# Kernel tuning notes

Measured on AMD Instinct MI355X. Metric: run time of the kernel, lower is better.

Reference implementation:

```python
import jax, jax.numpy as jnp
import numpy as np
from jax.scipy.linalg import solve_triangular

L_SUB = 16          # subarray length (init arg L)
DL = 0.05           # diagonal loading factor


def setup_inputs() -> dict:
    key = jax.random.key(0)
    k0, k1, k2 = jax.random.split(key, 3)
    B, C, NS, NZ, NX = 2, 128, 1024, 256, 128
    rf = jax.random.normal(k0, (B, C, NS), jnp.float32)
    t0 = jnp.zeros((B,), jnp.float32)
    d_tx = jax.random.uniform(k1, (B, NZ, NX), dtype=jnp.float32)
    d_rx = jax.random.uniform(k2, (C, NZ, NX), dtype=jnp.float32)
    fs = jnp.float32((NS - 1) / 2.0)   # keeps sample positions in [0, NS-1]
    f0 = jnp.float32(5.0)              # unused by forward (kept for signature parity)
    c0 = jnp.float32(1.0)
    apod = jnp.ones((C,), jnp.float32) # unused by forward
    return dict(rf=rf, t0=t0, d_tx=d_tx, d_rx=d_rx, fs=fs, f0=f0, c0=c0, apod=apod)


def _aligned_signals(rf, t0, d_tx, d_rx, fs, c0):
    """Bilinear (1-D linear) resample of rf at per-pixel delays.
    Equivalent to torch grid_sample(mode='bilinear', padding_mode='border',
    align_corners=True) where the grid x-coord is samples*2/(NS-1)-1."""
    B, C, NS = rf.shape
    _, NZ, NX = d_tx.shape
    # samples: [B, C, NZ, NX] fractional sample index into rf
    samples = fs * ((d_tx[:, None, :, :] + d_rx[None, :, :, :]) / c0
                    + t0[:, None, None, None])
    pos = jnp.clip(samples, 0.0, NS - 1.0)          # border padding
    i0 = jnp.floor(pos).astype(jnp.int32)
    i1 = jnp.minimum(i0 + 1, NS - 1)
    frac = pos - i0.astype(pos.dtype)
    sig = rf.reshape(B * C, NS)
    i0f = i0.reshape(B * C, NZ * NX)
    i1f = i1.reshape(B * C, NZ * NX)
    v0 = jnp.take_along_axis(sig, i0f, axis=1).reshape(B, C, NZ, NX)
    v1 = jnp.take_along_axis(sig, i1f, axis=1).reshape(B, C, NZ, NX)
    return v0 * (1.0 - frac) + v1 * frac


def reference(rf, t0, d_tx, d_rx, fs, f0, c0, apod):
    B, C, NS = rf.shape
    _, NZ, NX = d_tx.shape
    M = C - L_SUB + 1  # number of subarrays (113)
    aligned = _aligned_signals(rf, t0, d_tx, d_rx, fs, c0)  # [B, C, NZ, NX]
    # per-pixel channel vectors: [P, C], P = B*NZ*NX
    xf = aligned.transpose(0, 2, 3, 1).reshape(-1, C)
    # subarray gather: S[p, m, l] = xf[p, m + l]  -> [P, M, L]
    idx = jnp.arange(M)[:, None] + jnp.arange(L_SUB)[None, :]
    S = xf[:, idx]
    # avg_pool1d(kernel=M, stride=1) over channels == mean over subarray axis
    x = S.mean(axis=1)                                  # [P, L]
    # spatially-smoothed covariance: R = S^T S / M, symmetrized
    R = jnp.einsum('pml,pmk->plk', S, S) / M
    R = 0.5 * (R + R.transpose(0, 2, 1))
    # diagonal loading: R += dl * (trace/L) * I
    delta = jnp.trace(R, axis1=-2, axis2=-1) / L_SUB    # [P]
    R = R + (DL * delta)[:, None, None] * jnp.eye(L_SUB, dtype=R.dtype)
    # Cholesky solve R u = 1
    Lc = jnp.linalg.cholesky(R)
    rhs = jnp.ones((R.shape[0], L_SUB, 1), R.dtype)
    y1 = solve_triangular(Lc, rhs, lower=True)
    u = solve_triangular(Lc, y1, lower=True, trans=1)[..., 0]  # [P, L]
    # MVDR weights (steering a = ones) and beamformed output
    denom = jnp.sum(u, axis=-1, keepdims=True) + 1e-10
    w = u / denom
    y = jnp.sum(w * x, axis=-1)                         # [P]
    return y.reshape(B, NZ, NX)
```

## Files before the change

kernel.cpp:

```cpp
#include <hip/hip_runtime.h>


namespace {

constexpr int kB  = 2;
constexpr int kC  = 128;
constexpr int kNS = 1024;
constexpr int kNZ = 256;
constexpr int kNX = 128;
constexpr int kZX = kNZ * kNX;
constexpr int kHalfC = 64;
constexpr int kRows = 4;
constexpr int kBufF = 2 * kRows * kNS;
constexpr int kTPB = 256;

__device__ __host__ constexpr int tri(int l, int k) {
  return l * 16 - (l * (l - 1)) / 2 + (k - l);
}

typedef __attribute__((address_space(1))) const void gconst_t;
typedef __attribute__((address_space(3))) void ldsv_t;

__device__ __forceinline__ void g2l16(const float* g, float* l) {
  __builtin_amdgcn_global_load_lds((gconst_t*)g, (ldsv_t*)l, 16, 0, 0);
}

__device__ __forceinline__ void stage_step(const float* __restrict__ rfb,
                                           float* tbuf, int q, int wave,
                                           int lane) {
  const int h = wave >> 1;
  const int woff = (wave & 1) * 2048;
  const float* gsrc = rfb + (size_t)(h * kHalfC + q * kRows) * kNS;
  float* ldst = tbuf + h * (kRows * kNS);
#pragma unroll
  for (int i = 0; i < 8; ++i)
    g2l16(gsrc + woff + i * 256 + lane * 4, ldst + woff + i * 256);
}

__device__ __forceinline__ void load_drx4(const float* __restrict__ drxp,
                                          int cbase, float (&d)[kRows]) {
#pragma unroll
  for (int r = 0; r < kRows; ++r)
    d[r] = drxp[(size_t)(cbase + r) * kZX];
}

template <int PH, bool HEAD>
__device__ __forceinline__ void compute4(
    const float* rows, const float (&drx)[kRows], float kk, float base,
    float (&F)[16], float (&win)[16], float (&head)[16], float& Sall) {
#pragma unroll
  for (int r = 0; r < kRows; ++r) {
    const int t = PH + r;
    float pos = fmaf(kk, drx[r], base);
    pos = fminf(fmaxf(pos, 0.0f), 1023.0f);
    int i0 = (int)pos;
    i0 = min(i0, kNS - 2);
    float frac = pos - (float)i0;
    const float* p = rows + r * kNS + i0;
    float v0 = p[0];
    float v1 = p[1];
    float v = fmaf(frac, v1 - v0, v0);
    Sall += v;
    F[0] = fmaf(v, v, F[0]);
    if constexpr (HEAD) {
#pragma unroll
      for (int d = 1; d <= t; ++d) F[d] = fmaf(v, win[t - d], F[d]);
      head[t] = v;
    } else {
#pragma unroll
      for (int d = 1; d < 16; ++d) F[d] = fmaf(v, win[(t - d) & 15], F[d]);
    }
    win[t] = v;
  }
}

#define STEP(Q, PH, HEADF, CUR, NXT)                                       \
  do {                                                                     \
    if ((Q) + 1 < 16) {                                                    \
      stage_step(rfb, tile[((Q) + 1) & 1], (Q) + 1, wave, lane);           \
      load_drx4(drxp, ((Q) + 1) * kRows, NXT);                             \
    }                                                                      \
    compute4<PH, HEADF>(tile[(Q) & 1] + half * (kRows * kNS), CUR, kk,     \
                        base, F, win, head, Sall);                         \
    __syncthreads();                                                       \
  } while (0)

__global__ __launch_bounds__(kTPB, 2) void mvb_fused_kernel(
    const float* __restrict__ rf, const float* __restrict__ t0,
    const float* __restrict__ d_tx, const float* __restrict__ d_rx,
    const float* __restrict__ fs_p, const float* __restrict__ c0_p,
    float* __restrict__ out) {
  __shared__ float tile[2][kBufF];

  const int tid = threadIdx.x;
  const int lane = tid & 63;
  const int wave = tid >> 6;
  const int half = tid >> 7;
  const int px = tid & 127;
  const int z = blockIdx.x & (kNZ - 1);
  const int b = blockIdx.x >> 8;
  const int pix = (int)((size_t)b * kZX + z * kNX + px);

  const float fs = fs_p[0];
  const float c0 = c0_p[0];
  const float kk = fs / c0;
  const float base = fs * (d_tx[pix] / c0 + t0[b]);

  const float* rfb = rf + (size_t)b * kC * kNS;
  const float* drxp =
      d_rx + (size_t)half * kHalfC * kZX + (size_t)z * kNX + px;

  float F[16], win[16], head[16];
  float Sall = 0.0f;
#pragma unroll
  for (int i = 0; i < 16; ++i) F[i] = 0.0f;

  float drxA[kRows], drxB[kRows];

  stage_step(rfb, tile[0], 0, wave, lane);
  load_drx4(drxp, 0, drxA);
  __syncthreads();

  STEP(0, 0, true, drxA, drxB);
  STEP(1, 4, true, drxB, drxA);
  STEP(2, 8, true, drxA, drxB);
  STEP(3, 12, true, drxB, drxA);
#pragma unroll 1
  for (int g = 1; g < 4; ++g) {
    const int q = g * 4;
    STEP(q + 0, 0, false, drxA, drxB);
    STEP(q + 1, 4, false, drxB, drxA);
    STEP(q + 2, 8, false, drxA, drxB);
    STEP(q + 3, 12, false, drxB, drxA);
  }

  float* xch = tile[0];
  if (half == 0) {
#pragma unroll
    for (int i = 0; i < 16; ++i) xch[i * 128 + px] = F[i];
#pragma unroll
    for (int i = 0; i < 16; ++i) xch[(16 + i) * 128 + px] = win[i];
#pragma unroll
    for (int i = 0; i < 16; ++i) xch[(32 + i) * 128 + px] = head[i];
    xch[48 * 128 + px] = Sall;
  }
  __syncthreads();
  if (half == 0) return;

  float hlo[16];
  {
    float wlo[16];
#pragma unroll
    for (int i = 0; i < 16; ++i) wlo[i] = xch[(16 + i) * 128 + px];
#pragma unroll
    for (int i = 0; i < 16; ++i) hlo[i] = xch[(32 + i) * 128 + px];
    Sall += xch[48 * 128 + px];
    F[0] += xch[0 * 128 + px];
#pragma unroll
    for (int d = 1; d < 16; ++d) {
      float s = xch[d * 128 + px];
#pragma unroll
      for (int i = 0; i < d; ++i) s = fmaf(head[i], wlo[16 - d + i], s);
      F[d] += s;
    }
  }

  float Ru[136];
#pragma unroll
  for (int d = 0; d < 16; ++d) {
    float t0s = 0.0f;
#pragma unroll
    for (int i = d + 1; i < 16; ++i) t0s = fmaf(win[i - d], win[i], t0s);
    Ru[tri(0, d)] = F[d] - t0s;
#pragma unroll
    for (int l = 1; l < 16 - d; ++l)
      Ru[tri(l, l + d)] = Ru[tri(l - 1, l - 1 + d)] -
                          hlo[l - 1] * hlo[l - 1 + d] +
                          win[l] * win[l + d];
  }

  float tr = 0.0f;
#pragma unroll
  for (int l = 0; l < 16; ++l) tr += Ru[tri(l, l)];
  const float dl = tr * (0.05f / 16.0f);
#pragma unroll
  for (int l = 0; l < 16; ++l) Ru[tri(l, l)] += dl;

  float X[16];
  {
    float s = Sall;
#pragma unroll
    for (int i = 1; i < 16; ++i) s -= win[i];
    X[0] = s;
#pragma unroll
    for (int l = 1; l < 16; ++l) X[l] = X[l - 1] - hlo[l - 1] + win[l];
  }

  float inv[16];
#pragma unroll
  for (int j = 0; j < 16; ++j) {
    float d = Ru[tri(j, j)];
#pragma unroll
    for (int p = 0; p < j; ++p) d = fmaf(-Ru[tri(p, j)], Ru[tri(p, j)], d);
    inv[j] = rsqrtf(d);
#pragma unroll
    for (int i = j + 1; i < 16; ++i) {
      float s = Ru[tri(j, i)];
#pragma unroll
      for (int p = 0; p < j; ++p) s = fmaf(-Ru[tri(p, i)], Ru[tri(p, j)], s);
      Ru[tri(j, i)] = s * inv[j];
    }
  }

  float yv[16];
#pragma unroll
  for (int i = 0; i < 16; ++i) {
    float s = 1.0f;
#pragma unroll
    for (int j = 0; j < i; ++j) s = fmaf(-Ru[tri(j, i)], yv[j], s);
    yv[i] = s * inv[i];
  }
  float u[16];
#pragma unroll
  for (int i = 15; i >= 0; --i) {
    float s = yv[i];
#pragma unroll
    for (int j = i + 1; j < 16; ++j) s = fmaf(-Ru[tri(i, j)], u[j], s);
    u[i] = s * inv[i];
  }

  float su = 0.0f, dot = 0.0f;
#pragma unroll
  for (int i = 0; i < 16; ++i) {
    su += u[i];
    dot = fmaf(u[i], X[i], dot);
  }
  out[pix] = dot / (113.0f * su + 1e-10f);
}

}

extern "C" void kernel_launch(void* const* d_in, const int* in_sizes, int n_in,
                              void* d_out, int out_size, void* d_ws,
                              size_t ws_size, hipStream_t stream) {
  const float* rf   = (const float*)d_in[0];
  const float* t0   = (const float*)d_in[1];
  const float* d_tx = (const float*)d_in[2];
  const float* d_rx = (const float*)d_in[3];
  const float* fs   = (const float*)d_in[4];
  const float* c0   = (const float*)d_in[6];
  float* out = (float*)d_out;

  hipLaunchKernelGGL(mvb_fused_kernel, dim3(kB * kNZ), dim3(kTPB), 0, stream,
                     rf, t0, d_tx, d_rx, fs, c0, out);
}
```

Before: 97.66 us.

## Replace block-wide double buffering with per-wave 4-deep LDS ring and waitcnt pipelining

Each wave now stages its own rf rows into a private 4-slot LDS ring using async global-to-LDS loads, three rows ahead. It synchronises with explicit vmcnt/lgkmcnt waits instead of a __syncthreads after every 4-row step. All 64 d_rx values are preloaded into registers up front. Launch bounds drop to 1 block per CU, trading occupancy and a larger register footprint for removing the per-step block barriers.

Result: slower. 100.7 us (+3.2%).

```diff
diff --git a/kernel.cpp b/kernel.cpp
--- a/kernel.cpp
+++ b/kernel.cpp
@@ -9,9 +9,6 @@
 constexpr int kNZ = 256;
 constexpr int kNX = 128;
 constexpr int kZX = kNZ * kNX;
-constexpr int kHalfC = 64;
-constexpr int kRows = 4;
-constexpr int kBufF = 2 * kRows * kNS;
 constexpr int kTPB = 256;
 
 __device__ __host__ constexpr int tri(int l, int k) {
@@ -25,140 +22,139 @@
   __builtin_amdgcn_global_load_lds((gconst_t*)g, (ldsv_t*)l, 16, 0, 0);
 }
 
-__device__ __forceinline__ void stage_step(const float* __restrict__ rfb,
-                                           float* tbuf, int q, int wave,
-                                           int lane) {
-  const int h = wave >> 1;
-  const int woff = (wave & 1) * 2048;
-  const float* gsrc = rfb + (size_t)(h * kHalfC + q * kRows) * kNS;
-  float* ldst = tbuf + h * (kRows * kNS);
-#pragma unroll
-  for (int i = 0; i < 8; ++i)
-    g2l16(gsrc + woff + i * 256 + lane * 4, ldst + woff + i * 256);
-}
-
-__device__ __forceinline__ void load_drx4(const float* __restrict__ drxp,
-                                          int cbase, float (&d)[kRows]) {
-#pragma unroll
-  for (int r = 0; r < kRows; ++r)
-    d[r] = drxp[(size_t)(cbase + r) * kZX];
-}
-
-template <int PH, bool HEAD>
-__device__ __forceinline__ void compute4(
-    const float* rows, const float (&drx)[kRows], float kk, float base,
-    float (&F)[16], float (&win)[16], float (&head)[16], float& Sall) {
-#pragma unroll
-  for (int r = 0; r < kRows; ++r) {
-    const int t = PH + r;
-    float pos = fmaf(kk, drx[r], base);
-    pos = fminf(fmaxf(pos, 0.0f), 1023.0f);
-    int i0 = (int)pos;
-    i0 = min(i0, kNS - 2);
-    float frac = pos - (float)i0;
-    const float* p = rows + r * kNS + i0;
-    float v0 = p[0];
-    float v1 = p[1];
-    float v = fmaf(frac, v1 - v0, v0);
-    Sall += v;
-    F[0] = fmaf(v, v, F[0]);
-    if constexpr (HEAD) {
-#pragma unroll
-      for (int d = 1; d <= t; ++d) F[d] = fmaf(v, win[t - d], F[d]);
-      head[t] = v;
-    } else {
-#pragma unroll
-      for (int d = 1; d < 16; ++d) F[d] = fmaf(v, win[(t - d) & 15], F[d]);
-    }
-    win[t] = v;
-  }
-}
-
-#define STEP(Q, PH, HEADF, CUR, NXT)                                       \
+__device__ __forceinline__ void stage1(const float* __restrict__ g, float* l,
+                                       int lane) {
+#pragma unroll
+  for (int j = 0; j < 4; ++j) g2l16(g + j * 256 + lane * 4, l + j * 256);
+}
+
+template <int T, bool HEAD>
+__device__ __forceinline__ void compute1(const float* row, float dr, float kk,
+                                         float base, float (&F)[16],
+                                         float (&win)[16], float (&head)[16],
+                                         float& Sall) {
+  float pos = fmaf(kk, dr, base);
+  pos = fminf(fmaxf(pos, 0.0f), 1023.0f);
+  int i0 = (int)pos;
+  i0 = min(i0, kNS - 2);
+  float frac = pos - (float)i0;
+  const float* p = row + i0;
+  float v0 = p[0];
+  float v1 = p[1];
+  float v = fmaf(frac, v1 - v0, v0);
+  Sall += v;
+  F[0] = fmaf(v, v, F[0]);
+  if constexpr (HEAD) {
+#pragma unroll
+    for (int d = 1; d <= T; ++d) F[d] = fmaf(v, win[T - d], F[d]);
+    head[T] = v;
+  } else {
+#pragma unroll
+    for (int d = 1; d < 16; ++d) F[d] = fmaf(v, win[(T - d) & 15], F[d]);
+  }
+  win[T] = v;
+}
+
+#define ST(I, WN, HEADF)                                                   \
   do {                                                                     \
-    if ((Q) + 1 < 16) {                                                    \
-      stage_step(rfb, tile[((Q) + 1) & 1], (Q) + 1, wave, lane);           \
-      load_drx4(drxp, ((Q) + 1) * kRows, NXT);                             \
+    if ((I) + 3 < 64) {                                                    \
+      asm volatile("s_waitcnt lgkmcnt(0)" ::: "memory");                   \
+      stage1(rfh + (size_t)((I) + 3) * kNS, ldsw + (((I) + 3) & 3) * 1024, \
+             lane);                                                        \
     }                                                                      \
-    compute4<PH, HEADF>(tile[(Q) & 1] + half * (kRows * kNS), CUR, kk,     \
-                        base, F, win, head, Sall);                         \
-    __syncthreads();                                                       \
+    asm volatile("s_waitcnt vmcnt(" #WN ")" ::: "memory");                 \
+    compute1<((I) & 15), (HEADF)>(ldsw + ((I) & 3) * 1024, drx[(I)], kk,   \
+                                  base, F, win, head, Sall);               \
   } while (0)
 
-__global__ __launch_bounds__(kTPB, 2) void mvb_fused_kernel(
+__global__ __launch_bounds__(kTPB, 1) void mvb_fused_kernel(
     const float* __restrict__ rf, const float* __restrict__ t0,
     const float* __restrict__ d_tx, const float* __restrict__ d_rx,
     const float* __restrict__ fs_p, const float* __restrict__ c0_p,
     float* __restrict__ out) {
-  __shared__ float tile[2][kBufF];
+  __shared__ float lds[4][4096];
 
   const int tid = threadIdx.x;
   const int lane = tid & 63;
   const int wave = tid >> 6;
-  const int half = tid >> 7;
-  const int px = tid & 127;
+  const int half = wave & 1;
+  const int grp = wave >> 1;
+  const int pxr = grp * 64 + lane;
   const int z = blockIdx.x & (kNZ - 1);
   const int b = blockIdx.x >> 8;
-  const int pix = (int)((size_t)b * kZX + z * kNX + px);
+  const int pix = (int)((size_t)b * kZX + z * kNX + pxr);
+  float* ldsw = &lds[wave][0];
 
   const float fs = fs_p[0];
   const float c0 = c0_p[0];
   const float kk = fs / c0;
   const float base = fs * (d_tx[pix] / c0 + t0[b]);
 
-  const float* rfb = rf + (size_t)b * kC * kNS;
+  const float* rfh = rf + (size_t)b * kC * kNS + (size_t)half * 64 * kNS;
   const float* drxp =
-      d_rx + (size_t)half * kHalfC * kZX + (size_t)z * kNX + px;
+      d_rx + (size_t)half * 64 * kZX + (size_t)z * kNX + pxr;
+
+  float drx[64];
+#pragma unroll
+  for (int c = 0; c < 64; ++c) drx[c] = drxp[(size_t)c * kZX];
 
   float F[16], win[16], head[16];
   float Sall = 0.0f;
 #pragma unroll
   for (int i = 0; i < 16; ++i) F[i] = 0.0f;
 
-  float drxA[kRows], drxB[kRows];
-
-  stage_step(rfb, tile[0], 0, wave, lane);
-  load_drx4(drxp, 0, drxA);
-  __syncthreads();
-
-  STEP(0, 0, true, drxA, drxB);
-  STEP(1, 4, true, drxB, drxA);
-  STEP(2, 8, true, drxA, drxB);
-  STEP(3, 12, true, drxB, drxA);
-#pragma unroll 1
-  for (int g = 1; g < 4; ++g) {
-    const int q = g * 4;
-    STEP(q + 0, 0, false, drxA, drxB);
-    STEP(q + 1, 4, false, drxB, drxA);
-    STEP(q + 2, 8, false, drxA, drxB);
-    STEP(q + 3, 12, false, drxB, drxA);
-  }
-
-  float* xch = tile[0];
+  asm volatile("s_waitcnt vmcnt(0)" ::: "memory");
+
+  stage1(rfh + 0 * kNS, ldsw + 0 * 1024, lane);
+  stage1(rfh + 1 * kNS, ldsw + 1 * 1024, lane);
+  stage1(rfh + 2 * kNS, ldsw + 2 * 1024, lane);
+
+  ST(0, 12, true);  ST(1, 12, true);  ST(2, 12, true);  ST(3, 12, true);
+  ST(4, 12, true);  ST(5, 12, true);  ST(6, 12, true);  ST(7, 12, true);
+  ST(8, 12, true);  ST(9, 12, true);  ST(10, 12, true); ST(11, 12, true);
+  ST(12, 12, true); ST(13, 12, true); ST(14, 12, true); ST(15, 12, true);
+
+  ST(16, 12, false); ST(17, 12, false); ST(18, 12, false); ST(19, 12, false);
+  ST(20, 12, false); ST(21, 12, false); ST(22, 12, false); ST(23, 12, false);
+  ST(24, 12, false); ST(25, 12, false); ST(26, 12, false); ST(27, 12, false);
+  ST(28, 12, false); ST(29, 12, false); ST(30, 12, false); ST(31, 12, false);
+
+  ST(32, 12, false); ST(33, 12, false); ST(34, 12, false); ST(35, 12, false);
+  ST(36, 12, false); ST(37, 12, false); ST(38, 12, false); ST(39, 12, false);
+  ST(40, 12, false); ST(41, 12, false); ST(42, 12, false); ST(43, 12, false);
+  ST(44, 12, false); ST(45, 12, false); ST(46, 12, false); ST(47, 12, false);
+
+  ST(48, 12, false); ST(49, 12, false); ST(50, 12, false); ST(51, 12, false);
+  ST(52, 12, false); ST(53, 12, false); ST(54, 12, false); ST(55, 12, false);
+  ST(56, 12, false); ST(57, 12, false); ST(58, 12, false); ST(59, 12, false);
+  ST(60, 12, false); ST(61, 8, false);  ST(62, 4, false);  ST(63, 0, false);
+
   if (half == 0) {
-#pragma unroll
-    for (int i = 0; i < 16; ++i) xch[i * 128 + px] = F[i];
-#pragma unroll
-    for (int i = 0; i < 16; ++i) xch[(16 + i) * 128 + px] = win[i];
-#pragma unroll
-    for (int i = 0; i < 16; ++i) xch[(32 + i) * 128 + px] = head[i];
-    xch[48 * 128 + px] = Sall;
+    float* xo = &lds[wave][0];
+#pragma unroll
+    for (int i = 0; i < 16; ++i) xo[i * 64 + lane] = F[i];
+#pragma unroll
+    for (int i = 0; i < 16; ++i) xo[(16 + i) * 64 + lane] = win[i];
+#pragma unroll
+    for (int i = 0; i < 16; ++i) xo[(32 + i) * 64 + lane] = head[i];
+    xo[48 * 64 + lane] = Sall;
   }
   __syncthreads();
   if (half == 0) return;
 
+  const float* xch = &lds[wave ^ 1][0];
   float hlo[16];
   {
     float wlo[16];
 #pragma unroll
-    for (int i = 0; i < 16; ++i) wlo[i] = xch[(16 + i) * 128 + px];
-#pragma unroll
-    for (int i = 0; i < 16; ++i) hlo[i] = xch[(32 + i) * 128 + px];
-    Sall += xch[48 * 128 + px];
-    F[0] += xch[0 * 128 + px];
+    for (int i = 0; i < 16; ++i) wlo[i] = xch[(16 + i) * 64 + lane];
+#pragma unroll
+    for (int i = 0; i < 16; ++i) hlo[i] = xch[(32 + i) * 64 + lane];
+    Sall += xch[48 * 64 + lane];
+    F[0] += xch[0 * 64 + lane];
 #pragma unroll
     for (int d = 1; d < 16; ++d) {
-      float s = xch[d * 128 + px];
+      float s = xch[d * 64 + lane];
 #pragma unroll
       for (int i = 0; i < d; ++i) s = fmaf(head[i], wlo[16 - d + i], s);
       F[d] += s;
```
